# Optimization experiments

Hardware: AMD Instinct MI355X
Metric: run time of the kernel (lower is better)

The kernel has to match this reference:

```python
import jax, jax.numpy as jnp
import numpy as np

K = 2          # diffusion steps
HID = 64       # hidden_dim
T_OUT = 12     # decoder horizon
EPS = 1e-6


def _random_walk(A):
    # W_fwd = D_out^{-1} A ; W_bwd = D_in^{-1} A^T  (row-normalized)
    W_fwd = A / (A.sum(axis=1, keepdims=True) + EPS)
    AT = A.T
    W_bwd = AT / (AT.sum(axis=1, keepdims=True) + EPS)
    return W_fwd, W_bwd


def _dconv(xin, Wf, Wb, W, b):
    # xin: (B, N, F). K forward + K backward random-walk hops, concat, linear.
    outs = [xin]
    xf = xin
    for _ in range(K):
        xf = jnp.einsum('ij,bjf->bif', Wf, xf)
        outs.append(xf)
    xb = xin
    for _ in range(K):
        xb = jnp.einsum('ij,bjf->bif', Wb, xb)
        outs.append(xb)
    return jnp.concatenate(outs, axis=-1) @ W + b


def _cell(xl, h, Wr, br, Wz, bz, Wn, bn, Wf, Wb):
    xh = jnp.concatenate([xl, h], axis=-1)
    r = jax.nn.sigmoid(_dconv(xh, Wf, Wb, Wr, br))
    z = jax.nn.sigmoid(_dconv(xh, Wf, Wb, Wz, bz))
    xrh = jnp.concatenate([xl, r * h], axis=-1)
    n = jnp.tanh(_dconv(xrh, Wf, Wb, Wn, bn))
    return (1.0 - z) * h + z * n


def setup_inputs() -> dict:
    key = jax.random.key(0)
    ks = jax.random.split(key, 20)
    B, T_in, N = 16, 12, 512
    x = jax.random.normal(ks[0], (B, T_in, N), dtype=jnp.float32)
    A = jax.random.uniform(ks[1], (N, N), dtype=jnp.float32)

    def lin(k, fan_in, fan_out):
        s = 1.0 / np.sqrt(fan_in)
        kw, kb = jax.random.split(k)
        W = jax.random.uniform(kw, (fan_in, fan_out), jnp.float32, -s, s)
        b = jax.random.uniform(kb, (fan_out,), jnp.float32, -s, s)
        return W, b

    in0 = (2 * K + 1) * (1 + HID)    # 325
    in1 = (2 * K + 1) * (2 * HID)    # 640
    Wr0, br0 = lin(ks[2], in0, HID)
    Wz0, bz0 = lin(ks[3], in0, HID)
    Wn0, bn0 = lin(ks[4], in0, HID)
    Wr1, br1 = lin(ks[5], in1, HID)
    Wz1, bz1 = lin(ks[6], in1, HID)
    Wn1, bn1 = lin(ks[7], in1, HID)
    Wp, bp = lin(ks[8], HID, 1)
    return dict(x=x, A=A, Wr0=Wr0, br0=br0, Wz0=Wz0, bz0=bz0, Wn0=Wn0, bn0=bn0,
                Wr1=Wr1, br1=br1, Wz1=Wz1, bz1=bz1, Wn1=Wn1, bn1=bn1, Wp=Wp, bp=bp)


def reference(x, A, Wr0, br0, Wz0, bz0, Wn0, bn0,
              Wr1, br1, Wz1, bz1, Wn1, bn1, Wp, bp):
    Wf, Wb = _random_walk(A)
    B, T_in, N = x.shape
    x4 = x[..., None]                             # (B, T_in, N, 1)
    h0 = jnp.zeros((B, N, HID), x.dtype)
    h1 = jnp.zeros((B, N, HID), x.dtype)

    def enc_step(carry, xt):
        h0, h1 = carry
        h0 = _cell(xt, h0, Wr0, br0, Wz0, bz0, Wn0, bn0, Wf, Wb)
        h1 = _cell(h0, h1, Wr1, br1, Wz1, bz1, Wn1, bn1, Wf, Wb)
        return (h0, h1), None

    (h0, h1), _ = jax.lax.scan(enc_step, (h0, h1), jnp.moveaxis(x4, 1, 0))

    def dec_step(carry, _):
        h0, h1, di = carry
        h0 = _cell(di, h0, Wr0, br0, Wz0, bz0, Wn0, bn0, Wf, Wb)
        h1 = _cell(h0, h1, Wr1, br1, Wz1, bz1, Wn1, bn1, Wf, Wb)
        yt = h1 @ Wp + bp                          # (B, N, 1)
        return (h0, h1, yt), yt

    (_, _, _), ys = jax.lax.scan(dec_step, (h0, h1, x4[:, -1]), None, length=T_OUT)
    return jnp.moveaxis(ys, 0, 1)[..., 0]          # (B, T_out, N)
```

## Files before the change

kernel.cpp:

```cpp
#include <hip/hip_runtime.h>
#include <math.h>

#define T_IN   12
#define T_OUT  12
#define NB     8192
#define EPSV   1e-6f

typedef __attribute__((ext_vector_type(8))) short short8;
typedef __attribute__((ext_vector_type(4))) float floatx4;

__device__ __forceinline__ unsigned short f2bf(float x) {
    union { float f; unsigned u; } v; v.f = x;
    unsigned r = v.u + 0x7fffu + ((v.u >> 16) & 1u);
    return (unsigned short)(r >> 16);
}
__device__ __forceinline__ float bf2f(unsigned short h) {
    union { float f; unsigned u; } v; v.u = ((unsigned)h) << 16;
    return v.f;
}
__device__ __forceinline__ unsigned packbf(float v) {
    unsigned u = __float_as_uint(v);
    unsigned hu = u & 0xffff0000u;
    float r = v - __uint_as_float(hu);
    unsigned ru = __float_as_uint(r);
    return (ru & 0xffff0000u) | (u >> 16);
}
__device__ __forceinline__ void split2(float v, short& h, short& l) {
    unsigned u = __float_as_uint(v);
    h = (short)(u >> 16);
    float r = v - __uint_as_float(u & 0xffff0000u);
    l = (short)(__float_as_uint(r) >> 16);
}

__device__ __forceinline__ float sigmoid_fast(float x) {
    return 1.0f / (1.0f + __expf(-x));
}
__device__ __forceinline__ float tanh_fast(float x) {
    float e = __expf(2.0f * x);
    return 1.0f - 2.0f / (e + 1.0f);
}

struct HopA {
    const float* M[4];
    float* dst0[4];
};

struct HopM {
    const unsigned short* Ahi[4]; const unsigned short* Alo[4];
    const unsigned* src0; const unsigned* src1;
    unsigned* dst0[4]; unsigned* dst1[4];
    int tiles0;
};

struct XHopM {
    const unsigned short* Ahi[4]; const unsigned short* Alo[4];
    const float* X;
    float* Y;
    int ncols;
};

struct WPack { const float* w[4]; unsigned short* hi[4]; unsigned short* lo[4]; };

struct LPack {
    const float* W; unsigned short* hi; unsigned short* lo;
    int base[10]; int nseg;
};

struct LinA {
    const unsigned* seg[10]; int nseg;
    const float* sx[5]; int sxrow[5]; int nsx;
};

__global__ void sums_kernel(const float* __restrict__ A, float* __restrict__ rs,
                            float* __restrict__ cs) {
    int i = blockIdx.x;
    int t = threadIdx.x;
    __shared__ float s1[256], s2[256];
    float a = A[i * 512 + t] + A[i * 512 + t + 256];
    float b = A[t * 512 + i] + A[(t + 256) * 512 + i];
    s1[t] = a; s2[t] = b;
    __syncthreads();
    for (int off = 128; off > 0; off >>= 1) {
        if (t < off) { s1[t] += s1[t + off]; s2[t] += s2[t + off]; }
        __syncthreads();
    }
    if (t == 0) { rs[i] = s1[0]; cs[i] = s2[0]; }
}

__global__ void fill_kernel(const float* __restrict__ A, const float* __restrict__ rs,
                            const float* __restrict__ cs, float* __restrict__ Wf,
                            float* __restrict__ Wb) {
    int i = blockIdx.x;
    float irs = 1.0f / (rs[i] + EPSV);
    float ics = 1.0f / (cs[i] + EPSV);
    for (int j = threadIdx.x; j < 512; j += 256) {
        Wf[i * 512 + j] = A[i * 512 + j] * irs;
        Wb[i * 512 + j] = A[j * 512 + i] * ics;
    }
}

__global__ void xenc_kernel(const float* __restrict__ x, float* __restrict__ xenc) {
    int idx = blockIdx.x * 256 + threadIdx.x;
    if (idx >= T_IN * NB) return;
    int j = idx & 511;
    int b = (idx >> 9) & 15;
    int t = idx >> 13;
    xenc[t * NB + j * 16 + b] = x[(b * T_IN + t) * 512 + j];
}

__global__ __launch_bounds__(256) void ghop_kernel(HopA a) {
    int z = blockIdx.z;
    const float* Wm = a.M[z];
    const float* X = Wm;
    float* Y = a.dst0[z];
    int col0 = blockIdx.x * 64;
    int row0 = blockIdx.y * 64;
    int tid = threadIdx.x;
    int tx = tid & 15, ty = tid >> 4;
    int kkA = tid & 15, rrA = tid >> 4;
    int ccB = tid & 63, kkB = tid >> 6;

    __shared__ float As[16][68], Bs[16][68];
    float acc[4][4] = {};

    const float* wp = Wm + (row0 + rrA) * 512 + kkA;
    const float* xp = X + (size_t)(col0 + ccB) + (size_t)kkB * 512;

    float ra[4], rb[4];
#pragma unroll
    for (int p = 0; p < 4; ++p) ra[p] = wp[p * 16 * 512];
#pragma unroll
    for (int p = 0; p < 4; ++p) rb[p] = xp[(size_t)(p * 4) * 512];

    for (int k0 = 0; k0 < 512; k0 += 16) {
#pragma unroll
        for (int p = 0; p < 4; ++p) As[kkA][rrA + p * 16] = ra[p];
#pragma unroll
        for (int p = 0; p < 4; ++p) Bs[kkB + p * 4][ccB] = rb[p];
        __syncthreads();
        if (k0 + 16 < 512) {
            int kn = k0 + 16;
#pragma unroll
            for (int p = 0; p < 4; ++p) ra[p] = wp[p * 16 * 512 + kn];
#pragma unroll
            for (int p = 0; p < 4; ++p) rb[p] = xp[(size_t)(kn + p * 4) * 512];
        }
#pragma unroll
        for (int k = 0; k < 16; ++k) {
            const float4 a4 = *(const float4*)&As[k][ty * 4];
            const float4 b4 = *(const float4*)&Bs[k][tx * 4];
            float av[4] = { a4.x, a4.y, a4.z, a4.w };
            float bv[4] = { b4.x, b4.y, b4.z, b4.w };
#pragma unroll
            for (int i = 0; i < 4; ++i)
#pragma unroll
                for (int j = 0; j < 4; ++j)
                    acc[i][j] = fmaf(av[i], bv[j], acc[i][j]);
        }
        __syncthreads();
    }

    int colw = col0 + tx * 4;
#pragma unroll
    for (int i = 0; i < 4; ++i) {
        int row = row0 + ty * 4 + i;
        *(float4*)&Y[(size_t)row * 512 + colw] =
            make_float4(acc[i][0], acc[i][1], acc[i][2], acc[i][3]);
    }
}

__global__ void wpack_kernel(WPack a) {
    int z = blockIdx.y;
    int idx = blockIdx.x * 256 + threadIdx.x;
    int m = idx >> 9, k = idx & 511;
    float x = a.w[z][idx];
    unsigned short h = f2bf(x);
    unsigned short l = f2bf(x - bf2f(h));
    int p = (((m >> 4) * 64 + (k >> 3)) * 16 + (m & 15)) * 8 + (k & 7);
    a.hi[z][p] = h;
    a.lo[z][p] = l;
}

__global__ void lpack_kernel(LPack p) {
    int idx = blockIdx.x * 256 + threadIdx.x;
    if (idx >= p.nseg * 4096) return;
    int j = idx & 7, ln = (idx >> 3) & 15, ntl = (idx >> 7) & 3, O = idx >> 9;
    int s = O >> 3, o8 = O & 7;
    int row = p.base[s] + o8 * 8 + j;
    int col = ntl * 16 + ln;
    float v = p.W[(size_t)row * 64 + col];
    unsigned short h = f2bf(v);
    p.hi[idx] = h;
    p.lo[idx] = f2bf(v - bf2f(h));
}

template<int MI>
__global__ __launch_bounds__(256) void hop_mfma(HopM a) {
    int z = blockIdx.z;
    int nt = blockIdx.x;
    const unsigned* X; unsigned* Y; int c0;
    if (nt < a.tiles0) { X = a.src0; Y = a.dst0[z]; c0 = nt * 64; }
    else { X = a.src1; Y = a.dst1[z]; c0 = (nt - a.tiles0) * 64; }
    const unsigned short* Ahi = a.Ahi[z];
    const unsigned short* Alo = a.Alo[z];
    int bm = blockIdx.y * (MI * 32);

    __shared__ unsigned short Bhi_s[2][64][40];
    __shared__ unsigned short Blo_s[2][64][40];

    int tid = threadIdx.x;
    int lane = tid & 63, w = tid >> 6;
    int wm = (w & 1) * (MI * 16), wn = (w >> 1) * 32;
    int ln = lane & 15, quad = lane >> 4;
    int sc = tid & 63, skh = tid >> 6;

    floatx4 acc[MI][2];
#pragma unroll
    for (int mi = 0; mi < MI; ++mi)
#pragma unroll
        for (int ci = 0; ci < 2; ++ci) acc[mi][ci] = (floatx4)0.0f;

    const unsigned* xbase = X + c0 + sc;
    int mtb = (bm + wm) >> 4;

    unsigned uv[8];
#pragma unroll
    for (int j = 0; j < 8; ++j)
        uv[j] = xbase[(size_t)(skh * 8 + j) * 1024];
    {
        short8 h8, l8;
#pragma unroll
        for (int j = 0; j < 8; ++j) {
            h8[j] = (short)(uv[j] & 0xffffu);
            l8[j] = (short)(uv[j] >> 16);
        }
        *(short8*)&Bhi_s[0][sc][skh * 8] = h8;
        *(short8*)&Blo_s[0][sc][skh * 8] = l8;
    }
#pragma unroll
    for (int j = 0; j < 8; ++j)
        uv[j] = xbase[(size_t)(32 + skh * 8 + j) * 1024];

    for (int it = 0; it < 16; ++it) {
        __syncthreads();
        int cur = it & 1;
        if (it + 1 < 16) {
            short8 h8, l8;
#pragma unroll
            for (int j = 0; j < 8; ++j) {
                h8[j] = (short)(uv[j] & 0xffffu);
                l8[j] = (short)(uv[j] >> 16);
            }
            *(short8*)&Bhi_s[cur ^ 1][sc][skh * 8] = h8;
            *(short8*)&Blo_s[cur ^ 1][sc][skh * 8] = l8;
        }
        if (it + 2 < 16) {
            int kn = (it + 2) * 32;
#pragma unroll
            for (int j = 0; j < 8; ++j)
                uv[j] = xbase[(size_t)(kn + skh * 8 + j) * 1024];
        }
        short8 bh[2], bl[2];
#pragma unroll
        for (int ci = 0; ci < 2; ++ci) {
            bh[ci] = *(const short8*)&Bhi_s[cur][wn + ci * 16 + ln][quad * 8];
            bl[ci] = *(const short8*)&Blo_s[cur][wn + ci * 16 + ln][quad * 8];
        }
        int kob = it * 4 + quad;
#pragma unroll
        for (int mi = 0; mi < MI; ++mi) {
            size_t aoff = ((size_t)((mtb + mi) * 64 + kob) * 16 + ln) * 8;
            short8 Ah = *(const short8*)(Ahi + aoff);
            short8 Al = *(const short8*)(Alo + aoff);
#pragma unroll
            for (int ci = 0; ci < 2; ++ci) {
                acc[mi][ci] = __builtin_amdgcn_mfma_f32_16x16x32_bf16(Ah, bh[ci], acc[mi][ci], 0, 0, 0);
                acc[mi][ci] = __builtin_amdgcn_mfma_f32_16x16x32_bf16(Ah, bl[ci], acc[mi][ci], 0, 0, 0);
                acc[mi][ci] = __builtin_amdgcn_mfma_f32_16x16x32_bf16(Al, bh[ci], acc[mi][ci], 0, 0, 0);
            }
        }
    }

#pragma unroll
    for (int mi = 0; mi < MI; ++mi) {
#pragma unroll
        for (int ci = 0; ci < 2; ++ci) {
            int mrow = bm + wm + mi * 16 + quad * 4;
            int col = c0 + wn + ci * 16 + ln;
#pragma unroll
            for (int r = 0; r < 4; ++r)
                Y[(size_t)(mrow + r) * 1024 + col] = packbf(acc[mi][ci][r]);
        }
    }
}

__global__ __launch_bounds__(256) void xhop_mfma(XHopM a) {
    int z = blockIdx.z;
    int c0 = blockIdx.x * 64;
    const unsigned short* Ahi = a.Ahi[z];
    const unsigned short* Alo = a.Alo[z];
    int bm = blockIdx.y * 64;

    __shared__ unsigned short Bhi_s[2][64][40];
    __shared__ unsigned short Blo_s[2][64][40];

    int tid = threadIdx.x;
    int lane = tid & 63, w = tid >> 6;
    int wm = (w & 1) * 32, wn = (w >> 1) * 32;
    int ln = lane & 15, quad = lane >> 4;
    int sc = tid & 63, skh = tid >> 6;

    floatx4 acc[2][2];
#pragma unroll
    for (int mi = 0; mi < 2; ++mi)
#pragma unroll
        for (int ci = 0; ci < 2; ++ci) acc[mi][ci] = (floatx4)0.0f;

    int colS = c0 + sc;
    bool ok = colS < a.ncols;
    const float* xb = a.X + (size_t)(colS >> 4) * NB + (colS & 15);
    int mtb = (bm + wm) >> 4;

    float xv[8];
#pragma unroll
    for (int j = 0; j < 8; ++j)
        xv[j] = ok ? xb[(size_t)(skh * 8 + j) * 16] : 0.0f;
    {
        short8 h8, l8;
#pragma unroll
        for (int j = 0; j < 8; ++j) { short h, l; split2(xv[j], h, l); h8[j] = h; l8[j] = l; }
        *(short8*)&Bhi_s[0][sc][skh * 8] = h8;
        *(short8*)&Blo_s[0][sc][skh * 8] = l8;
    }
#pragma unroll
    for (int j = 0; j < 8; ++j)
        xv[j] = ok ? xb[(size_t)(32 + skh * 8 + j) * 16] : 0.0f;

    for (int it = 0; it < 16; ++it) {
        __syncthreads();
        int cur = it & 1;
        if (it + 1 < 16) {
            short8 h8, l8;
#pragma unroll
            for (int j = 0; j < 8; ++j) { short h, l; split2(xv[j], h, l); h8[j] = h; l8[j] = l; }
            *(short8*)&Bhi_s[cur ^ 1][sc][skh * 8] = h8;
            *(short8*)&Blo_s[cur ^ 1][sc][skh * 8] = l8;
        }
        if (it + 2 < 16) {
            int kn = (it + 2) * 32;
#pragma unroll
            for (int j = 0; j < 8; ++j)
                xv[j] = ok ? xb[(size_t)(kn + skh * 8 + j) * 16] : 0.0f;
        }
        short8 bh[2], bl[2];
#pragma unroll
        for (int ci = 0; ci < 2; ++ci) {
            bh[ci] = *(const short8*)&Bhi_s[cur][wn + ci * 16 + ln][quad * 8];
            bl[ci] = *(const short8*)&Blo_s[cur][wn + ci * 16 + ln][quad * 8];
        }
        int kob = it * 4 + quad;
#pragma unroll
        for (int mi = 0; mi < 2; ++mi) {
            size_t aoff = ((size_t)((mtb + mi) * 64 + kob) * 16 + ln) * 8;
            short8 Ah = *(const short8*)(Ahi + aoff);
            short8 Al = *(const short8*)(Alo + aoff);
#pragma unroll
            for (int ci = 0; ci < 2; ++ci) {
                acc[mi][ci] = __builtin_amdgcn_mfma_f32_16x16x32_bf16(Ah, bh[ci], acc[mi][ci], 0, 0, 0);
                acc[mi][ci] = __builtin_amdgcn_mfma_f32_16x16x32_bf16(Ah, bl[ci], acc[mi][ci], 0, 0, 0);
                acc[mi][ci] = __builtin_amdgcn_mfma_f32_16x16x32_bf16(Al, bh[ci], acc[mi][ci], 0, 0, 0);
            }
        }
    }

#pragma unroll
    for (int mi = 0; mi < 2; ++mi) {
#pragma unroll
        for (int ci = 0; ci < 2; ++ci) {
            int col = c0 + wn + ci * 16 + ln;
            if (col < a.ncols) {
                int mrow = bm + wm + mi * 16 + quad * 4;
                float* yb = a.Y + (size_t)((col >> 4) * 4 + z) * NB + (col & 15);
#pragma unroll
                for (int r = 0; r < 4; ++r)
                    yb[(size_t)(mrow + r) * 16] = acc[mi][ci][r];
            }
        }
    }
}

__device__ __forceinline__ void lin_core2(const unsigned* const* segs, int nseg, int s0,
        const unsigned short* __restrict__ Bh, const unsigned short* __restrict__ Bl,
        int row0, int ln, int quad, int cihalf, floatx4 acc[2]) {
    for (int s = 0; s < nseg; ++s) {
        const unsigned* ap = segs[s] + (size_t)(row0 + ln) * 64 + quad * 8;
#pragma unroll
        for (int hh = 0; hh < 2; ++hh) {
            unsigned u[8];
            *(uint4*)&u[0] = *(const uint4*)(ap + hh * 32);
            *(uint4*)&u[4] = *(const uint4*)(ap + hh * 32 + 4);
            short8 Ah, Al;
#pragma unroll
            for (int j = 0; j < 8; ++j) {
                Ah[j] = (short)(u[j] & 0xffffu);
                Al[j] = (short)(u[j] >> 16);
            }
            int O = (s0 + s) * 8 + hh * 4 + quad;
#pragma unroll
            for (int ci = 0; ci < 2; ++ci) {
                int c_abs = cihalf * 2 + ci;
                size_t boff = ((size_t)(O * 4 + c_abs) * 16 + ln) * 8;
                short8 B1 = *(const short8*)(Bh + boff);
                short8 B2 = *(const short8*)(Bl + boff);
                acc[ci] = __builtin_amdgcn_mfma_f32_16x16x32_bf16(Ah, B1, acc[ci], 0, 0, 0);
                acc[ci] = __builtin_amdgcn_mfma_f32_16x16x32_bf16(Al, B1, acc[ci], 0, 0, 0);
                acc[ci] = __builtin_amdgcn_mfma_f32_16x16x32_bf16(Ah, B2, acc[ci], 0, 0, 0);
            }
        }
    }
}

__device__ __forceinline__ void lin_scalar2(const LinA& a, const float* __restrict__ WO,
        int row0, int ln, int quad, int cihalf, floatx4 acc[2]) {
    for (int t = 0; t < a.nsx; ++t) {
        const float* wr = WO + (size_t)a.sxrow[t] * 64;
        const float* sv = a.sx[t] + row0 + quad * 4;
#pragma unroll
        for (int rr = 0; rr < 4; ++rr) {
            float v = sv[rr];
#pragma unroll
            for (int ci = 0; ci < 2; ++ci)
                acc[ci][rr] = fmaf(v, wr[(cihalf * 2 + ci) * 16 + ln], acc[ci][rr]);
        }
    }
}

__global__ __launch_bounds__(256) void lin_rz_mfma(
    LinA a,
    const unsigned short* Wrh, const unsigned short* Wrl, const float* WrO, const float* br,
    const unsigned short* Wzh, const unsigned short* Wzl, const float* WzO, const float* bz,
    const float* __restrict__ h, unsigned* __restrict__ GP, float* __restrict__ Z) {
    int w = threadIdx.x >> 6, lane = threadIdx.x & 63;
    int ln = lane & 15, quad = lane >> 4;
    int row0 = blockIdx.x * 64 + w * 16;
    int gate = blockIdx.y;
    int cihalf = blockIdx.z;
    const unsigned short* Bh = gate ? Wzh : Wrh;
    const unsigned short* Bl = gate ? Wzl : Wrl;
    const float* WO = gate ? WzO : WrO;
    const float* bias = gate ? bz : br;
    floatx4 acc[2];
    acc[0] = (floatx4)0.0f; acc[1] = (floatx4)0.0f;
    lin_core2(a.seg, a.nseg, 0, Bh, Bl, row0, ln, quad, cihalf, acc);
    if (a.nsx) lin_scalar2(a, WO, row0, ln, quad, cihalf, acc);
#pragma unroll
    for (int ci = 0; ci < 2; ++ci) {
        int col = (cihalf * 2 + ci) * 16 + ln;
        float bv = bias[col];
#pragma unroll
        for (int rr = 0; rr < 4; ++rr) {
            int row = row0 + quad * 4 + rr;
            size_t idx = (size_t)row * 64 + col;
            float sg = sigmoid_fast(acc[ci][rr] + bv);
            if (gate == 0) GP[idx] = packbf(sg * h[idx]);
            else Z[idx] = sg;
        }
    }
}

__global__ __launch_bounds__(256) void lin_n_mfma(
    LinA a, int ksplit,
    const unsigned short* Wnh, const unsigned short* Wnl,
    const float* WnO, const float* bn,
    const float* __restrict__ Zb, float* __restrict__ h, unsigned* __restrict__ hP,
    int doProj, const float* __restrict__ Wp, const float* __restrict__ bp,
    float* __restrict__ out, float* __restrict__ di, int t) {
    int w = threadIdx.x >> 6, lane = threadIdx.x & 63;
    int ln = lane & 15, quad = lane >> 4;
    int kh = w & 1, cihalf = w >> 1;
    int row0 = blockIdx.x * 16;
    __shared__ float part[2][2][16][17];
    __shared__ float pr[2][16];
    floatx4 acc[2];
    acc[0] = (floatx4)0.0f; acc[1] = (floatx4)0.0f;
    if (kh == 0) {
        lin_core2(a.seg, ksplit, 0, Wnh, Wnl, row0, ln, quad, cihalf, acc);
    } else {
        lin_core2(a.seg + ksplit, a.nseg - ksplit, ksplit, Wnh, Wnl, row0, ln, quad, cihalf, acc);
        if (a.nsx) lin_scalar2(a, WnO, row0, ln, quad, cihalf, acc);
#pragma unroll
        for (int ci = 0; ci < 2; ++ci)
#pragma unroll
            for (int rr = 0; rr < 4; ++rr)
                part[cihalf][ci][quad * 4 + rr][ln] = acc[ci][rr];
    }
    __syncthreads();
    float p[4] = {0.0f, 0.0f, 0.0f, 0.0f};
    if (kh == 0) {
#pragma unroll
        for (int ci = 0; ci < 2; ++ci) {
            int col = (cihalf * 2 + ci) * 16 + ln;
            float bv = bn[col];
            float wpv = doProj ? Wp[col] : 0.0f;
#pragma unroll
            for (int rr = 0; rr < 4; ++rr) {
                int row = row0 + quad * 4 + rr;
                size_t idx = (size_t)row * 64 + col;
                float pre = acc[ci][rr] + part[cihalf][ci][quad * 4 + rr][ln] + bv;
                float nn = tanh_fast(pre);
                float z = Zb[idx];
                float hv = h[idx];
                float o = (1.0f - z) * hv + z * nn;
                h[idx] = o;
                hP[idx] = packbf(o);
                p[rr] = fmaf(o, wpv, p[rr]);
            }
        }
        if (doProj) {
#pragma unroll
            for (int rr = 0; rr < 4; ++rr) {
                p[rr] += __shfl_xor(p[rr], 1, 64);
                p[rr] += __shfl_xor(p[rr], 2, 64);
                p[rr] += __shfl_xor(p[rr], 4, 64);
                p[rr] += __shfl_xor(p[rr], 8, 64);
            }
            if (ln == 0) {
#pragma unroll
                for (int rr = 0; rr < 4; ++rr)
                    pr[cihalf][quad * 4 + rr] = p[rr];
            }
        }
    }
    __syncthreads();
    if (doProj && kh == 0 && cihalf == 0 && ln == 0) {
        float bpv = bp[0];
#pragma unroll
        for (int rr = 0; rr < 4; ++rr) {
            int qr = quad * 4 + rr;
            int row = row0 + qr;
            float y = pr[0][qr] + pr[1][qr] + bpv;
            int n = row >> 4, b = row & 15;
            out[(b * T_OUT + t) * 512 + n] = y;
            di[row] = y;
        }
    }
}

extern "C" void kernel_launch(void* const* d_in, const int* in_sizes, int n_in,
                              void* d_out, int out_size, void* d_ws, size_t ws_size,
                              hipStream_t stream) {
    (void)in_sizes; (void)n_in; (void)out_size; (void)ws_size;
    const float* x   = (const float*)d_in[0];
    const float* A   = (const float*)d_in[1];
    const float* Wr0 = (const float*)d_in[2];  const float* br0 = (const float*)d_in[3];
    const float* Wz0 = (const float*)d_in[4];  const float* bz0 = (const float*)d_in[5];
    const float* Wn0 = (const float*)d_in[6];  const float* bn0 = (const float*)d_in[7];
    const float* Wr1 = (const float*)d_in[8];  const float* br1 = (const float*)d_in[9];
    const float* Wz1 = (const float*)d_in[10]; const float* bz1 = (const float*)d_in[11];
    const float* Wn1 = (const float*)d_in[12]; const float* bn1 = (const float*)d_in[13];
    const float* Wp  = (const float*)d_in[14]; const float* bp  = (const float*)d_in[15];
    float* out = (float*)d_out;

    float* ws = (float*)d_ws;
    size_t off = 0;
    auto alloc = [&](size_t nf) { float* p = ws + off; off += nf; return p; };
    float* Wf  = alloc(262144); float* Wb  = alloc(262144);
    float* W2f = alloc(262144); float* W2b = alloc(262144);
    float* rs  = alloc(512);    float* cs  = alloc(512);
    float* xenc = alloc((size_t)T_IN * NB);
    unsigned short* Whi[4]; unsigned short* Wlo[4];
    for (int m = 0; m < 4; ++m) Whi[m] = (unsigned short*)alloc(131072);
    for (int m = 0; m < 4; ++m) Wlo[m] = (unsigned short*)alloc(131072);
    unsigned* HAall = (unsigned*)alloc(4 * 524288);
    unsigned* HA_P[4]; for (int m = 0; m < 4; ++m) HA_P[m] = HAall + (size_t)m * 524288;
    unsigned* HB_P[4]; unsigned* HG_P[4];
    for (int m = 0; m < 4; ++m) HB_P[m] = (unsigned*)alloc(524288);
    for (int m = 0; m < 4; ++m) HG_P[m] = (unsigned*)alloc(524288);
    unsigned* GP  = (unsigned*)alloc(524288);
    unsigned* h0P = (unsigned*)alloc(524288);
    unsigned* h1P = (unsigned*)alloc(524288);
    float* Z  = alloc(524288);
    float* h0 = alloc(524288);
    float* h1 = alloc(524288);
    float* XHE = alloc((size_t)T_IN * 4 * NB);
    float* HXSdec = alloc(4 * NB);
    float* di = alloc(NB);
    unsigned short* LWh[6]; unsigned short* LWl[6];
    for (int g = 0; g < 3; ++g) { LWh[g] = (unsigned short*)alloc(10240); LWl[g] = (unsigned short*)alloc(10240); }
    for (int g = 3; g < 6; ++g) { LWh[g] = (unsigned short*)alloc(20480); LWl[g] = (unsigned short*)alloc(20480); }

    hipMemsetAsync(h0, 0, 524288 * sizeof(float), stream);
    hipMemsetAsync(h1, 0, 524288 * sizeof(float), stream);
    hipMemsetAsync(h0P, 0, 524288 * sizeof(unsigned), stream);
    hipMemsetAsync(h1P, 0, 524288 * sizeof(unsigned), stream);
    hipMemsetAsync(HAall, 0, 4ul * 524288 * sizeof(unsigned), stream);

    xenc_kernel<<<dim3((T_IN * NB) / 256), 256, 0, stream>>>(x, xenc);
    sums_kernel<<<dim3(512), 256, 0, stream>>>(A, rs, cs);
    fill_kernel<<<dim3(512), 256, 0, stream>>>(A, rs, cs, Wf, Wb);

    {
        HopA w2 = {};
        w2.M[0] = Wf; w2.M[1] = Wb;
        w2.dst0[0] = W2f; w2.dst0[1] = W2b;
        ghop_kernel<<<dim3(8, 8, 2), 256, 0, stream>>>(w2);
    }
    {
        WPack p;
        p.w[0] = Wf; p.w[1] = W2f; p.w[2] = Wb; p.w[3] = W2b;
        for (int m = 0; m < 4; ++m) { p.hi[m] = Whi[m]; p.lo[m] = Wlo[m]; }
        wpack_kernel<<<dim3(1024, 4), 256, 0, stream>>>(p);
    }
    {
        const float* WG[6] = { Wr0, Wz0, Wn0, Wr1, Wz1, Wn1 };
        for (int g = 0; g < 6; ++g) {
            LPack p = {};
            p.W = WG[g]; p.hi = LWh[g]; p.lo = LWl[g];
            if (g < 3) { p.nseg = 5;  for (int s = 0; s < 5; ++s)  p.base[s] = 65 * s + 1; }
            else       { p.nseg = 10; for (int s = 0; s < 10; ++s) p.base[s] = 64 * s; }
            lpack_kernel<<<dim3((p.nseg * 4096 + 255) / 256), 256, 0, stream>>>(p);
        }
    }
    {
        XHopM xa = {};
        for (int m = 0; m < 4; ++m) { xa.Ahi[m] = Whi[m]; xa.Alo[m] = Wlo[m]; }
        xa.X = xenc; xa.Y = XHE; xa.ncols = 192;
        xhop_mfma<<<dim3(3, 8, 4), 256, 0, stream>>>(xa);
    }

    auto hopcom = [&](HopM& a) {
        for (int m = 0; m < 4; ++m) { a.Ahi[m] = Whi[m]; a.Alo[m] = Wlo[m]; }
    };

    for (int t = 0; t < T_IN + T_OUT; ++t) {
        int dec = (t >= T_IN);
        int td = t - T_IN;
        const float* xcur; const float* hxs;
        if (!dec) { xcur = xenc + (size_t)t * NB; hxs = XHE + (size_t)t * 4 * NB; }
        else if (td == 0) { xcur = xenc + (size_t)(T_IN - 1) * NB; hxs = XHE + (size_t)(T_IN - 1) * 4 * NB; }
        else {
            xcur = di; hxs = HXSdec;
            XHopM xo = {};
            for (int m = 0; m < 4; ++m) { xo.Ahi[m] = Whi[m]; xo.Alo[m] = Wlo[m]; }
            xo.X = di; xo.Y = HXSdec; xo.ncols = 16;
            xhop_mfma<<<dim3(1, 8, 4), 256, 0, stream>>>(xo);
        }

        LinA la = {};
        la.nseg = 5;
        la.seg[0] = h0P;
        for (int m = 0; m < 4; ++m) la.seg[1 + m] = HA_P[m];
        la.nsx = 5;
        la.sx[0] = xcur; la.sxrow[0] = 0;
        for (int m = 0; m < 4; ++m) { la.sx[1 + m] = hxs + (size_t)m * NB; la.sxrow[1 + m] = 65 * (m + 1); }
        lin_rz_mfma<<<dim3(128, 2, 2), 256, 0, stream>>>(la, LWh[0], LWl[0], Wr0, br0,
                                                         LWh[1], LWl[1], Wz0, bz0, h0, GP, Z);
        {
            HopM a = {}; hopcom(a);
            a.src0 = GP; a.tiles0 = 16;
            for (int m = 0; m < 4; ++m) a.dst0[m] = HG_P[m];
            hop_mfma<1><<<dim3(16, 16, 4), 256, 0, stream>>>(a);
        }
        LinA lb = la;
        lb.seg[0] = GP;
        for (int m = 0; m < 4; ++m) lb.seg[1 + m] = HG_P[m];
        lin_n_mfma<<<dim3(512), 256, 0, stream>>>(lb, 3, LWh[2], LWl[2], Wn0, bn0, Z, h0, h0P,
                                                  0, (const float*)nullptr, (const float*)nullptr,
                                                  (float*)nullptr, (float*)nullptr, 0);

        {
            HopM a = {}; hopcom(a);
            a.src0 = h0P; a.tiles0 = 16;
            a.src1 = h1P;
            for (int m = 0; m < 4; ++m) { a.dst0[m] = HA_P[m]; a.dst1[m] = HB_P[m]; }
            hop_mfma<2><<<dim3(32, 8, 4), 256, 0, stream>>>(a);
        }
        LinA lc = {};
        lc.nseg = 10; lc.nsx = 0;
        lc.seg[0] = h0P; lc.seg[1] = h1P;
        for (int m = 0; m < 4; ++m) { lc.seg[2 + 2 * m] = HA_P[m]; lc.seg[3 + 2 * m] = HB_P[m]; }
        lin_rz_mfma<<<dim3(128, 2, 2), 256, 0, stream>>>(lc, LWh[3], LWl[3], Wr1, br1,
                                                         LWh[4], LWl[4], Wz1, bz1, h1, GP, Z);
        {
            HopM a = {}; hopcom(a);
            a.src0 = GP; a.tiles0 = 16;
            for (int m = 0; m < 4; ++m) a.dst0[m] = HG_P[m];
            hop_mfma<1><<<dim3(16, 16, 4), 256, 0, stream>>>(a);
        }
        LinA ld = lc;
        ld.seg[1] = GP;
        for (int m = 0; m < 4; ++m) ld.seg[3 + 2 * m] = HG_P[m];
        lin_n_mfma<<<dim3(512), 256, 0, stream>>>(ld, 5, LWh[5], LWl[5], Wn1, bn1, Z, h1, h1P,
                                                  dec, Wp, bp, out, di, td);
    }
}
```

Measured before the change: 2.963 ms.

## Skew layer-0 of next step with layer-1 of current step into merged launches

Restructures the time loop so layer 0 of step t+1 runs in the same kernel launches as layer 1 of step t, since both depend only on h0 of step t. The r/z, graph-hop and n-gate kernels take two job descriptors and split the grid between them, roughly halving the number of serialized launches and filling the GPU better. Decoder steps use a new finish0 kernel that folds the scalar decoder-input hop into the r/z gate epilogue, and h0 is double-buffered. Setup kernels are also merged (sums+fill, six lpack launches into one). In exchange there is more complex indexing, extra buffers, and a risk of subtle ordering bugs.

```diff
diff --git a/kernel.cpp b/kernel.cpp
--- a/kernel.cpp
+++ b/kernel.cpp
@@ -61,18 +61,38 @@
 
 struct WPack { const float* w[4]; unsigned short* hi[4]; unsigned short* lo[4]; };
 
-struct LPack {
-    const float* W; unsigned short* hi; unsigned short* lo;
-    int base[10]; int nseg;
-};
-
-struct LinA {
+struct LPackAll { const float* W[6]; unsigned short* hi[6]; unsigned short* lo[6]; };
+
+struct LinJob {
     const unsigned* seg[10]; int nseg;
     const float* sx[5]; int sxrow[5]; int nsx;
+    const unsigned short* Wh[2]; const unsigned short* Wl[2];
+    const float* WO[2]; const float* bias[2];
+    const float* h; unsigned* GP; float* Z;
+    float* PR;
+    int mode;
 };
 
-__global__ void sums_kernel(const float* __restrict__ A, float* __restrict__ rs,
-                            float* __restrict__ cs) {
+struct NJob {
+    const unsigned* seg[10]; int nseg; int ksplit;
+    const float* sx[5]; int sxrow[5]; int nsx;
+    const unsigned short* Wh; const unsigned short* Wl;
+    const float* WO; const float* bias;
+    const float* Zb; const float* hin; float* hout; unsigned* hPout;
+    int doProj; const float* Wp; const float* bp; float* out; float* di; int t;
+};
+
+struct F0 {
+    const float* M[4];
+    const float* di;
+    const float* PR;
+    const float* WO[2]; const float* bias[2];
+    const float* h0;
+    unsigned* GP0; float* Z0; float* HXS;
+};
+
+__global__ void sumfill_kernel(const float* __restrict__ A, float* __restrict__ Wf,
+                               float* __restrict__ Wb) {
     int i = blockIdx.x;
     int t = threadIdx.x;
     __shared__ float s1[256], s2[256];
@@ -84,16 +104,9 @@
         if (t < off) { s1[t] += s1[t + off]; s2[t] += s2[t + off]; }
         __syncthreads();
     }
-    if (t == 0) { rs[i] = s1[0]; cs[i] = s2[0]; }
-}
-
-__global__ void fill_kernel(const float* __restrict__ A, const float* __restrict__ rs,
-                            const float* __restrict__ cs, float* __restrict__ Wf,
-                            float* __restrict__ Wb) {
-    int i = blockIdx.x;
-    float irs = 1.0f / (rs[i] + EPSV);
-    float ics = 1.0f / (cs[i] + EPSV);
-    for (int j = threadIdx.x; j < 512; j += 256) {
+    float irs = 1.0f / (s1[0] + EPSV);
+    float ics = 1.0f / (s2[0] + EPSV);
+    for (int j = t; j < 512; j += 256) {
         Wf[i * 512 + j] = A[i * 512 + j] * irs;
         Wb[i * 512 + j] = A[j * 512 + i] * ics;
     }
@@ -181,20 +194,22 @@
     a.lo[z][p] = l;
 }
 
-__global__ void lpack_kernel(LPack p) {
+__global__ void lpack_all_kernel(LPackAll p) {
+    int g = blockIdx.y;
+    int nseg = (g < 3) ? 5 : 10;
     int idx = blockIdx.x * 256 + threadIdx.x;
-    if (idx >= p.nseg * 4096) return;
+    if (idx >= nseg * 4096) return;
     int j = idx & 7, ln = (idx >> 3) & 15, ntl = (idx >> 7) & 3, O = idx >> 9;
     int s = O >> 3, o8 = O & 7;
-    int row = p.base[s] + o8 * 8 + j;
+    int base = (g < 3) ? (65 * s + 1) : (64 * s);
+    int row = base + o8 * 8 + j;
     int col = ntl * 16 + ln;
-    float v = p.W[(size_t)row * 64 + col];
+    float v = p.W[g][(size_t)row * 64 + col];
     unsigned short h = f2bf(v);
-    p.hi[idx] = h;
-    p.lo[idx] = f2bf(v - bf2f(h));
-}
-
-template<int MI>
+    p.hi[g][idx] = h;
+    p.lo[g][idx] = f2bf(v - bf2f(h));
+}
+
 __global__ __launch_bounds__(256) void hop_mfma(HopM a) {
     int z = blockIdx.z;
     int nt = blockIdx.x;
@@ -203,20 +218,20 @@
     else { X = a.src1; Y = a.dst1[z]; c0 = (nt - a.tiles0) * 64; }
     const unsigned short* Ahi = a.Ahi[z];
     const unsigned short* Alo = a.Alo[z];
-    int bm = blockIdx.y * (MI * 32);
+    int bm = blockIdx.y * 64;
 
     __shared__ unsigned short Bhi_s[2][64][40];
     __shared__ unsigned short Blo_s[2][64][40];
 
     int tid = threadIdx.x;
     int lane = tid & 63, w = tid >> 6;
-    int wm = (w & 1) * (MI * 16), wn = (w >> 1) * 32;
+    int wm = (w & 1) * 32, wn = (w >> 1) * 32;
     int ln = lane & 15, quad = lane >> 4;
     int sc = tid & 63, skh = tid >> 6;
 
-    floatx4 acc[MI][2];
-#pragma unroll
-    for (int mi = 0; mi < MI; ++mi)
+    floatx4 acc[2][2];
+#pragma unroll
+    for (int mi = 0; mi < 2; ++mi)
 #pragma unroll
         for (int ci = 0; ci < 2; ++ci) acc[mi][ci] = (floatx4)0.0f;
 
@@ -268,7 +283,7 @@
         }
         int kob = it * 4 + quad;
 #pragma unroll
-        for (int mi = 0; mi < MI; ++mi) {
+        for (int mi = 0; mi < 2; ++mi) {
             size_t aoff = ((size_t)((mtb + mi) * 64 + kob) * 16 + ln) * 8;
             short8 Ah = *(const short8*)(Ahi + aoff);
             short8 Al = *(const short8*)(Alo + aoff);
@@ -282,7 +297,7 @@
     }
 
 #pragma unroll
-    for (int mi = 0; mi < MI; ++mi) {
+    for (int mi = 0; mi < 2; ++mi) {
 #pragma unroll
         for (int ci = 0; ci < 2; ++ci) {
             int mrow = bm + wm + mi * 16 + quad * 4;
@@ -420,11 +435,12 @@
     }
 }
 
-__device__ __forceinline__ void lin_scalar2(const LinA& a, const float* __restrict__ WO,
+__device__ __forceinline__ void lin_scalar2p(const float* const* sx, const int* sxrow,
+        int nsx, const float* __restrict__ WO,
         int row0, int ln, int quad, int cihalf, floatx4 acc[2]) {
-    for (int t = 0; t < a.nsx; ++t) {
-        const float* wr = WO + (size_t)a.sxrow[t] * 64;
-        const float* sv = a.sx[t] + row0 + quad * 4;
+    for (int t = 0; t < nsx; ++t) {
+        const float* wr = WO + (size_t)sxrow[t] * 64;
+        const float* sv = sx[t] + row0 + quad * 4;
 #pragma unroll
         for (int rr = 0; rr < 4; ++rr) {
             float v = sv[rr];
@@ -435,59 +451,66 @@
     }
 }
 
-__global__ __launch_bounds__(256) void lin_rz_mfma(
-    LinA a,
-    const unsigned short* Wrh, const unsigned short* Wrl, const float* WrO, const float* br,
-    const unsigned short* Wzh, const unsigned short* Wzl, const float* WzO, const float* bz,
-    const float* __restrict__ h, unsigned* __restrict__ GP, float* __restrict__ Z) {
+__global__ __launch_bounds__(256) void lin_rz2(LinJob j0, LinJob j1, int xsplit) {
+    bool second = (int)blockIdx.x >= xsplit;
+    const LinJob& J = second ? j1 : j0;
+    int bx = (int)blockIdx.x - (second ? xsplit : 0);
     int w = threadIdx.x >> 6, lane = threadIdx.x & 63;
     int ln = lane & 15, quad = lane >> 4;
-    int row0 = blockIdx.x * 64 + w * 16;
+    int row0 = bx * 64 + w * 16;
     int gate = blockIdx.y;
     int cihalf = blockIdx.z;
-    const unsigned short* Bh = gate ? Wzh : Wrh;
-    const unsigned short* Bl = gate ? Wzl : Wrl;
-    const float* WO = gate ? WzO : WrO;
-    const float* bias = gate ? bz : br;
     floatx4 acc[2];
     acc[0] = (floatx4)0.0f; acc[1] = (floatx4)0.0f;
-    lin_core2(a.seg, a.nseg, 0, Bh, Bl, row0, ln, quad, cihalf, acc);
-    if (a.nsx) lin_scalar2(a, WO, row0, ln, quad, cihalf, acc);
-#pragma unroll
-    for (int ci = 0; ci < 2; ++ci) {
-        int col = (cihalf * 2 + ci) * 16 + ln;
-        float bv = bias[col];
-#pragma unroll
-        for (int rr = 0; rr < 4; ++rr) {
-            int row = row0 + quad * 4 + rr;
-            size_t idx = (size_t)row * 64 + col;
-            float sg = sigmoid_fast(acc[ci][rr] + bv);
-            if (gate == 0) GP[idx] = packbf(sg * h[idx]);
-            else Z[idx] = sg;
-        }
-    }
-}
-
-__global__ __launch_bounds__(256) void lin_n_mfma(
-    LinA a, int ksplit,
-    const unsigned short* Wnh, const unsigned short* Wnl,
-    const float* WnO, const float* bn,
-    const float* __restrict__ Zb, float* __restrict__ h, unsigned* __restrict__ hP,
-    int doProj, const float* __restrict__ Wp, const float* __restrict__ bp,
-    float* __restrict__ out, float* __restrict__ di, int t) {
+    lin_core2(J.seg, J.nseg, 0, J.Wh[gate], J.Wl[gate], row0, ln, quad, cihalf, acc);
+    if (J.nsx) lin_scalar2p(J.sx, J.sxrow, J.nsx, J.WO[gate], row0, ln, quad, cihalf, acc);
+    if (J.mode == 0) {
+        const float* bias = J.bias[gate];
+#pragma unroll
+        for (int ci = 0; ci < 2; ++ci) {
+            int col = (cihalf * 2 + ci) * 16 + ln;
+            float bv = bias[col];
+#pragma unroll
+            for (int rr = 0; rr < 4; ++rr) {
+                int row = row0 + quad * 4 + rr;
+                size_t idx = (size_t)row * 64 + col;
+                float sg = sigmoid_fast(acc[ci][rr] + bv);
+                if (gate == 0) J.GP[idx] = packbf(sg * J.h[idx]);
+                else J.Z[idx] = sg;
+            }
+        }
+    } else {
+        float* PRg = J.PR + (size_t)gate * ((size_t)NB * 64);
+#pragma unroll
+        for (int ci = 0; ci < 2; ++ci) {
+            int col = (cihalf * 2 + ci) * 16 + ln;
+#pragma unroll
+            for (int rr = 0; rr < 4; ++rr) {
+                int row = row0 + quad * 4 + rr;
+                PRg[(size_t)row * 64 + col] = acc[ci][rr];
+            }
+        }
+    }
+}
+
+__global__ __launch_bounds__(256) void lin_n2(NJob j0, NJob j1, int xsplit) {
+    bool second = (int)blockIdx.x >= xsplit;
+    const NJob& J = second ? j1 : j0;
+    int bx = (int)blockIdx.x - (second ? xsplit : 0);
     int w = threadIdx.x >> 6, lane = threadIdx.x & 63;
     int ln = lane & 15, quad = lane >> 4;
     int kh = w & 1, cihalf = w >> 1;
-    int row0 = blockIdx.x * 16;
+    int row0 = bx * 16;
     __shared__ float part[2][2][16][17];
     __shared__ float pr[2][16];
     floatx4 acc[2];
     acc[0] = (floatx4)0.0f; acc[1] = (floatx4)0.0f;
     if (kh == 0) {
-        lin_core2(a.seg, ksplit, 0, Wnh, Wnl, row0, ln, quad, cihalf, acc);
+        lin_core2(J.seg, J.ksplit, 0, J.Wh, J.Wl, row0, ln, quad, cihalf, acc);
     } else {
-        lin_core2(a.seg + ksplit, a.nseg - ksplit, ksplit, Wnh, Wnl, row0, ln, quad, cihalf, acc);
-        if (a.nsx) lin_scalar2(a, WnO, row0, ln, quad, cihalf, acc);
+        lin_core2(J.seg + J.ksplit, J.nseg - J.ksplit, J.ksplit, J.Wh, J.Wl,
+                  row0, ln, quad, cihalf, acc);
+        if (J.nsx) lin_scalar2p(J.sx, J.sxrow, J.nsx, J.WO, row0, ln, quad, cihalf, acc);
 #pragma unroll
         for (int ci = 0; ci < 2; ++ci)
 #pragma unroll
@@ -500,23 +523,23 @@
 #pragma unroll
         for (int ci = 0; ci < 2; ++ci) {
             int col = (cihalf * 2 + ci) * 16 + ln;
-            float bv = bn[col];
-            float wpv = doProj ? Wp[col] : 0.0f;
+            float bv = J.bias[col];
+            float wpv = J.doProj ? J.Wp[col] : 0.0f;
 #pragma unroll
             for (int rr = 0; rr < 4; ++rr) {
                 int row = row0 + quad * 4 + rr;
                 size_t idx = (size_t)row * 64 + col;
                 float pre = acc[ci][rr] + part[cihalf][ci][quad * 4 + rr][ln] + bv;
                 float nn = tanh_fast(pre);
-                float z = Zb[idx];
-                float hv = h[idx];
+                float z = J.Zb[idx];
+                float hv = J.hin[idx];
                 float o = (1.0f - z) * hv + z * nn;
-                h[idx] = o;
-                hP[idx] = packbf(o);
+                J.hout[idx] = o;
+                J.hPout[idx] = packbf(o);
                 p[rr] = fmaf(o, wpv, p[rr]);
             }
         }
-        if (doProj) {
+        if (J.doProj) {
 #pragma unroll
             for (int rr = 0; rr < 4; ++rr) {
                 p[rr] += __shfl_xor(p[rr], 1, 64);
@@ -532,17 +555,66 @@
         }
     }
     __syncthreads();
-    if (doProj && kh == 0 && cihalf == 0 && ln == 0) {
-        float bpv = bp[0];
+    if (J.doProj && kh == 0 && cihalf == 0 && ln == 0) {
+        float bpv = J.bp[0];
 #pragma unroll
         for (int rr = 0; rr < 4; ++rr) {
             int qr = quad * 4 + rr;
             int row = row0 + qr;
             float y = pr[0][qr] + pr[1][qr] + bpv;
             int n = row >> 4, b = row & 15;
-            out[(b * T_OUT + t) * 512 + n] = y;
-            di[row] = y;
-        }
+            J.out[(b * T_OUT + J.t) * 512 + n] = y;
+            J.di[row] = y;
+        }
+    }
+}
+
+__global__ __launch_bounds__(256) void finish0_kernel(F0 a) {
+    int b = blockIdx.x;
+    int tid = threadIdx.x;
+    int node_l = tid >> 6, m = (tid >> 4) & 3, bb = tid & 15;
+    int n = b * 4 + node_l;
+    int r0 = b * 64;
+    __shared__ float sh[4][4][16];
+    __shared__ float sdi[64];
+    if (tid < 64) sdi[tid] = a.di[r0 + tid];
+    const float* wrow = a.M[m] + (size_t)n * 512;
+    const float* dv = a.di + bb;
+    float s[8] = {};
+    for (int k = 0; k < 512; k += 8) {
+        float4 w0 = *(const float4*)&wrow[k];
+        float4 w1 = *(const float4*)&wrow[k + 4];
+        s[0] = fmaf(w0.x, dv[(k + 0) * 16], s[0]);
+        s[1] = fmaf(w0.y, dv[(k + 1) * 16], s[1]);
+        s[2] = fmaf(w0.z, dv[(k + 2) * 16], s[2]);
+        s[3] = fmaf(w0.w, dv[(k + 3) * 16], s[3]);
+        s[4] = fmaf(w1.x, dv[(k + 4) * 16], s[4]);
+        s[5] = fmaf(w1.y, dv[(k + 5) * 16], s[5]);
+        s[6] = fmaf(w1.z, dv[(k + 6) * 16], s[6]);
+        s[7] = fmaf(w1.w, dv[(k + 7) * 16], s[7]);
+    }
+    float dot = ((s[0] + s[1]) + (s[2] + s[3])) + ((s[4] + s[5]) + (s[6] + s[7]));
+    a.HXS[(size_t)m * NB + n * 16 + bb] = dot;
+    sh[node_l][m][bb] = dot;
+    __syncthreads();
+    int rloc = tid >> 2;
+    int cg = tid & 3;
+    int row = r0 + rloc;
+    int nl = rloc >> 4, bl = rloc & 15;
+    float dval = sdi[rloc];
+    for (int cc = 0; cc < 16; ++cc) {
+        int col = cg * 16 + cc;
+        size_t idx = (size_t)row * 64 + col;
+        float pre0 = a.PR[idx] + a.bias[0][col] + dval * a.WO[0][col];
+        float pre1 = a.PR[(size_t)NB * 64 + idx] + a.bias[1][col] + dval * a.WO[1][col];
+#pragma unroll
+        for (int mm = 0; mm < 4; ++mm) {
+            float hm = sh[nl][mm][bl];
+            pre0 = fmaf(hm, a.WO[0][(size_t)(65 * (mm + 1)) * 64 + col], pre0);
+            pre1 = fmaf(hm, a.WO[1][(size_t)(65 * (mm + 1)) * 64 + col], pre1);
+        }
+        a.GP0[idx] = packbf(sigmoid_fast(pre0) * a.h0[idx]);
+        a.Z0[idx] = sigmoid_fast(pre1);
     }
 }
 
@@ -564,24 +636,30 @@
     float* ws = (float*)d_ws;
     size_t off = 0;
     auto alloc = [&](size_t nf) { float* p = ws + off; off += nf; return p; };
+    const size_t NB64 = (size_t)NB * 64;
     float* Wf  = alloc(262144); float* Wb  = alloc(262144);
     float* W2f = alloc(262144); float* W2b = alloc(262144);
-    float* rs  = alloc(512);    float* cs  = alloc(512);
     float* xenc = alloc((size_t)T_IN * NB);
     unsigned short* Whi[4]; unsigned short* Wlo[4];
     for (int m = 0; m < 4; ++m) Whi[m] = (unsigned short*)alloc(131072);
     for (int m = 0; m < 4; ++m) Wlo[m] = (unsigned short*)alloc(131072);
-    unsigned* HAall = (unsigned*)alloc(4 * 524288);
-    unsigned* HA_P[4]; for (int m = 0; m < 4; ++m) HA_P[m] = HAall + (size_t)m * 524288;
-    unsigned* HB_P[4]; unsigned* HG_P[4];
-    for (int m = 0; m < 4; ++m) HB_P[m] = (unsigned*)alloc(524288);
-    for (int m = 0; m < 4; ++m) HG_P[m] = (unsigned*)alloc(524288);
-    unsigned* GP  = (unsigned*)alloc(524288);
-    unsigned* h0P = (unsigned*)alloc(524288);
-    unsigned* h1P = (unsigned*)alloc(524288);
-    float* Z  = alloc(524288);
-    float* h0 = alloc(524288);
-    float* h1 = alloc(524288);
+    unsigned* HAall = (unsigned*)alloc(4 * NB64);
+    unsigned* HBall = (unsigned*)alloc(4 * NB64);
+    unsigned* HA[4]; unsigned* HB[4]; unsigned* HG0[4]; unsigned* HG1[4];
+    for (int m = 0; m < 4; ++m) HA[m] = HAall + m * NB64;
+    for (int m = 0; m < 4; ++m) HB[m] = HBall + m * NB64;
+    for (int m = 0; m < 4; ++m) HG0[m] = (unsigned*)alloc(NB64);
+    for (int m = 0; m < 4; ++m) HG1[m] = (unsigned*)alloc(NB64);
+    unsigned* GP0 = (unsigned*)alloc(NB64);
+    unsigned* GP1 = (unsigned*)alloc(NB64);
+    float* Z0 = alloc(NB64);
+    float* Z1 = alloc(NB64);
+    float* h0x[2];  h0x[0] = alloc(NB64);  h0x[1] = alloc(NB64);
+    unsigned* h0Px[2];
+    h0Px[0] = (unsigned*)alloc(NB64); h0Px[1] = (unsigned*)alloc(NB64);
+    float* h1 = alloc(NB64);
+    unsigned* h1P = (unsigned*)alloc(NB64);
+    float* PR0 = alloc(2 * NB64);
     float* XHE = alloc((size_t)T_IN * 4 * NB);
     float* HXSdec = alloc(4 * NB);
     float* di = alloc(NB);
@@ -589,16 +667,15 @@
     for (int g = 0; g < 3; ++g) { LWh[g] = (unsigned short*)alloc(10240); LWl[g] = (unsigned short*)alloc(10240); }
     for (int g = 3; g < 6; ++g) { LWh[g] = (unsigned short*)alloc(20480); LWl[g] = (unsigned short*)alloc(20480); }
 
-    hipMemsetAsync(h0, 0, 524288 * sizeof(float), stream);
-    hipMemsetAsync(h1, 0, 524288 * sizeof(float), stream);
-    hipMemsetAsync(h0P, 0, 524288 * sizeof(unsigned), stream);
-    hipMemsetAsync(h1P, 0, 524288 * sizeof(unsigned), stream);
-    hipMemsetAsync(HAall, 0, 4ul * 524288 * sizeof(unsigned), stream);
+    hipMemsetAsync(h0x[1], 0, NB64 * 4, stream);
+    hipMemsetAsync(h0Px[1], 0, NB64 * 4, stream);
+    hipMemsetAsync(h1, 0, NB64 * 4, stream);
+    hipMemsetAsync(h1P, 0, NB64 * 4, stream);
+    hipMemsetAsync(HAall, 0, 4 * NB64 * 4, stream);
+    hipMemsetAsync(HBall, 0, 4 * NB64 * 4, stream);
 
     xenc_kernel<<<dim3((T_IN * NB) / 256), 256, 0, stream>>>(x, xenc);
-    sums_kernel<<<dim3(512), 256, 0, stream>>>(A, rs, cs);
-    fill_kernel<<<dim3(512), 256, 0, stream>>>(A, rs, cs, Wf, Wb);
-
+    sumfill_kernel<<<dim3(512), 256, 0, stream>>>(A, Wf, Wb);
     {
         HopA w2 = {};
         w2.M[0] = Wf; w2.M[1] = Wb;
@@ -612,14 +689,10 @@
         wpack_kernel<<<dim3(1024, 4), 256, 0, stream>>>(p);
     }
     {
+        LPackAll p;
         const float* WG[6] = { Wr0, Wz0, Wn0, Wr1, Wz1, Wn1 };
-        for (int g = 0; g < 6; ++g) {
-            LPack p = {};
-            p.W = WG[g]; p.hi = LWh[g]; p.lo = LWl[g];
-            if (g < 3) { p.nseg = 5;  for (int s = 0; s < 5; ++s)  p.base[s] = 65 * s + 1; }
-            else       { p.nseg = 10; for (int s = 0; s < 10; ++s) p.base[s] = 64 * s; }
-            lpack_kernel<<<dim3((p.nseg * 4096 + 255) / 256), 256, 0, stream>>>(p);
-        }
+        for (int g = 0; g < 6; ++g) { p.W[g] = WG[g]; p.hi[g] = LWh[g]; p.lo[g] = LWl[g]; }
+        lpack_all_kernel<<<dim3(160, 6), 256, 0, stream>>>(p);
     }
     {
         XHopM xa = {};
@@ -628,69 +701,112 @@
         xhop_mfma<<<dim3(3, 8, 4), 256, 0, stream>>>(xa);
     }
 
-    auto hopcom = [&](HopM& a) {
+    auto hopLaunch = [&](const unsigned* s0, unsigned* const* d0,
+                         const unsigned* s1, unsigned* const* d1) {
+        HopM a = {};
         for (int m = 0; m < 4; ++m) { a.Ahi[m] = Whi[m]; a.Alo[m] = Wlo[m]; }
+        a.src0 = s0; a.tiles0 = 16;
+        for (int m = 0; m < 4; ++m) a.dst0[m] = d0[m];
+        int tiles = 16;
+        if (s1) {
+            a.src1 = s1;
+            for (int m = 0; m < 4; ++m) a.dst1[m] = d1[m];
+            tiles = 32;
+        }
+        hop_mfma<<<dim3(tiles, 8, 4), 256, 0, stream>>>(a);
     };
 
+    auto mkRZ1 = [&](int t) {
+        LinJob J = {};
+        J.seg[0] = h0Px[t & 1]; J.seg[1] = h1P;
+        for (int m = 0; m < 4; ++m) { J.seg[2 + 2 * m] = HA[m]; J.seg[3 + 2 * m] = HB[m]; }
+        J.nseg = 10; J.nsx = 0;
+        J.Wh[0] = LWh[3]; J.Wl[0] = LWl[3]; J.Wh[1] = LWh[4]; J.Wl[1] = LWl[4];
+        J.WO[0] = Wr1; J.WO[1] = Wz1; J.bias[0] = br1; J.bias[1] = bz1;
+        J.h = h1; J.GP = GP1; J.Z = Z1; J.mode = 0;
+        return J;
+    };
+    auto mkRZ0 = [&](int tn, const float* xc, const float* hx, int mode) {
+        LinJob J = {};
+        J.seg[0] = h0Px[(tn - 1) & 1];
+        for (int m = 0; m < 4; ++m) J.seg[1 + m] = HA[m];
+        J.nseg = 5;
+        if (mode == 0) {
+            J.nsx = 5;
+            J.sx[0] = xc; J.sxrow[0] = 0;
+            for (int m = 0; m < 4; ++m) { J.sx[1 + m] = hx + (size_t)m * NB; J.sxrow[1 + m] = 65 * (m + 1); }
+        }
+        J.Wh[0] = LWh[0]; J.Wl[0] = LWl[0]; J.Wh[1] = LWh[1]; J.Wl[1] = LWl[1];
+        J.WO[0] = Wr0; J.WO[1] = Wz0; J.bias[0] = br0; J.bias[1] = bz0;
+        J.h = h0x[(tn - 1) & 1]; J.GP = GP0; J.Z = Z0; J.PR = PR0; J.mode = mode;
+        return J;
+    };
+    auto mkN1 = [&](int t) {
+        NJob J = {};
+        J.seg[0] = h0Px[t & 1]; J.seg[1] = GP1;
+        for (int m = 0; m < 4; ++m) { J.seg[2 + 2 * m] = HA[m]; J.seg[3 + 2 * m] = HG1[m]; }
+        J.nseg = 10; J.ksplit = 5; J.nsx = 0;
+        J.Wh = LWh[5]; J.Wl = LWl[5]; J.WO = Wn1; J.bias = bn1;
+        J.Zb = Z1; J.hin = h1; J.hout = h1; J.hPout = h1P;
+        J.doProj = (t >= T_IN); J.Wp = Wp; J.bp = bp; J.out = out; J.di = di; J.t = t - T_IN;
+        return J;
+    };
+    auto mkN0 = [&](int tn, const float* xc, const float* hx) {
+        NJob J = {};
+        J.seg[0] = GP0;
+        for (int m = 0; m < 4; ++m) J.seg[1 + m] = HG0[m];
+        J.nseg = 5; J.ksplit = 3;
+        J.nsx = 5;
+        J.sx[0] = xc; J.sxrow[0] = 0;
+        for (int m = 0; m < 4; ++m) { J.sx[1 + m] = hx + (size_t)m * NB; J.sxrow[1 + m] = 65 * (m + 1); }
+        J.Wh = LWh[2]; J.Wl = LWl[2]; J.WO = Wn0; J.bias = bn0;
+        J.Zb = Z0; J.hin = h0x[(tn - 1) & 1]; J.hout = h0x[tn & 1]; J.hPout = h0Px[tn & 1];
+        J.doProj = 0;
+        return J;
+    };
+
+    auto rz2one = [&](LinJob a) { lin_rz2<<<dim3(128, 2, 2), 256, 0, stream>>>(a, a, 128); };
+    auto rz2two = [&](LinJob a, LinJob b) { lin_rz2<<<dim3(256, 2, 2), 256, 0, stream>>>(a, b, 128); };
+    auto n2one = [&](NJob a) { lin_n2<<<dim3(512), 256, 0, stream>>>(a, a, 512); };
+    auto n2two = [&](NJob a, NJob b) { lin_n2<<<dim3(1024), 256, 0, stream>>>(a, b, 512); };
+
+    rz2one(mkRZ0(0, xenc, XHE, 0));
+    hopLaunch(GP0, HG0, nullptr, nullptr);
+    n2one(mkN0(0, xenc, XHE));
+    hopLaunch(h0Px[0], HA, nullptr, nullptr);
+
     for (int t = 0; t < T_IN + T_OUT; ++t) {
-        int dec = (t >= T_IN);
-        int td = t - T_IN;
-        const float* xcur; const float* hxs;
-        if (!dec) { xcur = xenc + (size_t)t * NB; hxs = XHE + (size_t)t * 4 * NB; }
-        else if (td == 0) { xcur = xenc + (size_t)(T_IN - 1) * NB; hxs = XHE + (size_t)(T_IN - 1) * 4 * NB; }
-        else {
-            xcur = di; hxs = HXSdec;
-            XHopM xo = {};
-            for (int m = 0; m < 4; ++m) { xo.Ahi[m] = Whi[m]; xo.Alo[m] = Wlo[m]; }
-            xo.X = di; xo.Y = HXSdec; xo.ncols = 16;
-            xhop_mfma<<<dim3(1, 8, 4), 256, 0, stream>>>(xo);
-        }
-
-        LinA la = {};
-        la.nseg = 5;
-        la.seg[0] = h0P;
-        for (int m = 0; m < 4; ++m) la.seg[1 + m] = HA_P[m];
-        la.nsx = 5;
-        la.sx[0] = xcur; la.sxrow[0] = 0;
-        for (int m = 0; m < 4; ++m) { la.sx[1 + m] = hxs + (size_t)m * NB; la.sxrow[1 + m] = 65 * (m + 1); }
-        lin_rz_mfma<<<dim3(128, 2, 2), 256, 0, stream>>>(la, LWh[0], LWl[0], Wr0, br0,
-                                                         LWh[1], LWl[1], Wz0, bz0, h0, GP, Z);
-        {
-            HopM a = {}; hopcom(a);
-            a.src0 = GP; a.tiles0 = 16;
-            for (int m = 0; m < 4; ++m) a.dst0[m] = HG_P[m];
-            hop_mfma<1><<<dim3(16, 16, 4), 256, 0, stream>>>(a);
-        }
-        LinA lb = la;
-        lb.seg[0] = GP;
-        for (int m = 0; m < 4; ++m) lb.seg[1 + m] = HG_P[m];
-        lin_n_mfma<<<dim3(512), 256, 0, stream>>>(lb, 3, LWh[2], LWl[2], Wn0, bn0, Z, h0, h0P,
-                                                  0, (const float*)nullptr, (const float*)nullptr,
-                                                  (float*)nullptr, (float*)nullptr, 0);
-
-        {
-            HopM a = {}; hopcom(a);
-            a.src0 = h0P; a.tiles0 = 16;
-            a.src1 = h1P;
-            for (int m = 0; m < 4; ++m) { a.dst0[m] = HA_P[m]; a.dst1[m] = HB_P[m]; }
-            hop_mfma<2><<<dim3(32, 8, 4), 256, 0, stream>>>(a);
-        }
-        LinA lc = {};
-        lc.nseg = 10; lc.nsx = 0;
-        lc.seg[0] = h0P; lc.seg[1] = h1P;
-        for (int m = 0; m < 4; ++m) { lc.seg[2 + 2 * m] = HA_P[m]; lc.seg[3 + 2 * m] = HB_P[m]; }
-        lin_rz_mfma<<<dim3(128, 2, 2), 256, 0, stream>>>(lc, LWh[3], LWl[3], Wr1, br1,
-                                                         LWh[4], LWl[4], Wz1, bz1, h1, GP, Z);
-        {
-            HopM a = {}; hopcom(a);
-            a.src0 = GP; a.tiles0 = 16;
-            for (int m = 0; m < 4; ++m) a.dst0[m] = HG_P[m];
-            hop_mfma<1><<<dim3(16, 16, 4), 256, 0, stream>>>(a);
-        }
-        LinA ld = lc;
-        ld.seg[1] = GP;
-        for (int m = 0; m < 4; ++m) ld.seg[3 + 2 * m] = HG_P[m];
-        lin_n_mfma<<<dim3(512), 256, 0, stream>>>(ld, 5, LWh[5], LWl[5], Wn1, bn1, Z, h1, h1P,
-                                                  dec, Wp, bp, out, di, td);
-    }
-}
+        int tn = t + 1;
+        bool last = (t == T_IN + T_OUT - 1);
+        bool decFeed = (tn >= T_IN + 1);
+        if (!last && !decFeed) {
+            int ts = (tn < T_IN) ? tn : (T_IN - 1);
+            const float* xc = xenc + (size_t)ts * NB;
+            const float* hx = XHE + (size_t)ts * 4 * NB;
+            rz2two(mkRZ1(t), mkRZ0(tn, xc, hx, 0));
+            hopLaunch(GP1, HG1, GP0, HG0);
+            n2two(mkN1(t), mkN0(tn, xc, hx));
+            hopLaunch(h0Px[tn & 1], HA, h1P, HB);
+        } else if (!last) {
+            rz2two(mkRZ1(t), mkRZ0(tn, nullptr, nullptr, 1));
+            hopLaunch(GP1, HG1, nullptr, nullptr);
+            n2one(mkN1(t));
+            {
+                F0 f = {};
+                f.M[0] = Wf; f.M[1] = W2f; f.M[2] = Wb; f.M[3] = W2b;
+                f.di = di; f.PR = PR0;
+                f.WO[0] = Wr0; f.WO[1] = Wz0; f.bias[0] = br0; f.bias[1] = bz0;
+                f.h0 = h0x[t & 1];
+                f.GP0 = GP0; f.Z0 = Z0; f.HXS = HXSdec;
+                finish0_kernel<<<dim3(128), 256, 0, stream>>>(f);
+            }
+            hopLaunch(GP0, HG0, nullptr, nullptr);
+            n2one(mkN0(tn, di, HXSdec));
+            hopLaunch(h0Px[tn & 1], HA, h1P, HB);
+        } else {
+            rz2one(mkRZ1(t));
+            hopLaunch(GP1, HG1, nullptr, nullptr);
+            n2one(mkN1(t));
+        }
+    }
+}
```

Result: slower. 4.500 ms (+51.9%).
